# Kernel tuning notes

Measured on AMD Instinct MI355X. Metric: run time of the kernel, lower is better.

The kernel has to match this reference:

```python
import jax, jax.numpy as jnp
import numpy as np
import math

B, T, E = 16, 4096, 1024
WIN = 15
EPS = 1e-6
HALF = T // 2


def _make_linear(key, out_f, in_f):
    k1, k2 = jax.random.split(key)
    lim = 1.0 / math.sqrt(in_f)
    W = jax.random.uniform(k1, (out_f, in_f), minval=-lim, maxval=lim, dtype=jnp.float32)
    b = jax.random.uniform(k2, (out_f,), minval=-lim, maxval=lim, dtype=jnp.float32)
    return W, b


def setup_inputs() -> dict:
    key = jax.random.key(0)
    ks = jax.random.split(key, 5)
    x = jax.random.normal(ks[0], (B, T, E), dtype=jnp.float32)
    taper = jnp.linspace(1.0, 0.0, T, dtype=jnp.float32)
    cW1, cb1 = _make_linear(ks[1], HALF, T)
    cW2, cb2 = _make_linear(ks[2], HALF, HALF)
    pW1, pb1 = _make_linear(ks[3], HALF, T)
    pW2, pb2 = _make_linear(ks[4], HALF, HALF)
    return {"x": x, "taper": taper,
            "cW1": cW1, "cb1": cb1, "cW2": cW2, "cb2": cb2,
            "pW1": pW1, "pb1": pb1, "pW2": pW2, "pb2": pb2}


def _compressor(h, W1, b1, W2, b2):
    # Linear -> SiLU -> Linear -> Tanh  (torch Linear: y = h @ W^T + b)
    h = jax.nn.silu(h @ W1.T + b1)
    return jnp.tanh(h @ W2.T + b2)


def _tdiff_raw(c0):
    Bb, Tt = c0.shape
    xp = jnp.pad(c0, ((0, 0), (WIN, 0)))  # left pad with zeros
    num = jnp.zeros_like(c0)
    for d in range(1, WIN + 1):  # small fixed loop over window lags
        num = num + float(d) * jax.lax.dynamic_slice_in_dim(xp, WIN - d, Tt, axis=1)
    i = jnp.arange(Tt, dtype=jnp.float32)
    s = jnp.minimum(i, float(WIN))
    norm = s * (s + 1.0) * 0.5
    return jnp.where(norm > 0, num / jnp.maximum(norm, 1.0), 0.0)


def reference(x, taper, cW1, cb1, cW2, cb2, pW1, pb1, pW2, pb2):
    x_t = x * taper[None, :, None]          # (B,T,E) tapered in time
    c0 = x_t[..., 0]                         # (B,T)
    r = jnp.abs(c0) + EPS
    start = jnp.where(c0 >= 0, 0.0, jnp.float32(math.pi))
    v = jnp.clip(x_t[..., 1:] / r[..., None], -1.0 + EPS, 1.0 - EPS)
    phases = start + jnp.arcsin(v).sum(axis=-1)  # (B,T)
    tdiff = _compressor(_tdiff_raw(c0), pW1, pb1, pW2, pb2)   # (B,T/2)
    thash = _compressor(phases, cW1, cb1, cW2, cb2)           # (B,T/2)
    return jnp.stack([thash, tdiff], axis=-1)                 # (B,T/2,2)
```

## Files before the change

kernel.cpp:

```cpp
#include <hip/hip_runtime.h>
#include <math.h>

#define BB 16
#define TT 4096
#define EE 1024
#define HALF 2048
#define WIN 15
#define EPSF 1e-6f
#define PI_F   3.14159265358979323846f
#define PIO2_F 1.57079632679489662f

__device__ __forceinline__ float fast_asinf(float v) {
    float a  = fabsf(v);
    float z1 = a * a;
    float z2 = 0.5f * (1.0f - a);
    bool big = a > 0.5f;
    float z = big ? z2 : z1;
    float s = big ? sqrtf(z) : a;
    float p = fmaf(z, 4.2163199048e-2f, 2.4181311049e-2f);
    p = fmaf(z, p, 4.5470025998e-2f);
    p = fmaf(z, p, 7.4953002686e-2f);
    p = fmaf(z, p, 1.6666752422e-1f);
    float r = fmaf(s * z, p, s);
    float rb = fmaf(-2.0f, r, PIO2_F);
    r = big ? rb : r;
    return copysignf(r, v);
}

__global__ void phase_kernel(const float* __restrict__ x,
                             const float* __restrict__ taper,
                             float* __restrict__ phases_b,
                             float* __restrict__ c0_b) {
    const int wave = threadIdx.x >> 6;
    const int lane = threadIdx.x & 63;
    const int row  = blockIdx.x * 4 + wave;
    const int b = row >> 12;
    const int t = row & (TT - 1);
    const float tap = taper[t];
    const float* xr = x + (size_t)row * EE;

    const float c0 = xr[0] * tap;
    const float r = fabsf(c0) + EPSF;
    const float scale = tap / r;
    const float start = (c0 >= 0.0f) ? 0.0f : PI_F;
    const float LO = -1.0f + EPSF, HI = 1.0f - EPSF;

    const float4* xr4 = (const float4*)xr;
    float sum = 0.0f;
    #pragma unroll
    for (int j = 0; j < 4; ++j) {
        float4 v = xr4[j * 64 + lane];
        float a0 = fast_asinf(fminf(fmaxf(v.x * scale, LO), HI));
        if ((j | lane) == 0) a0 = 0.0f;
        sum += a0;
        sum += fast_asinf(fminf(fmaxf(v.y * scale, LO), HI));
        sum += fast_asinf(fminf(fmaxf(v.z * scale, LO), HI));
        sum += fast_asinf(fminf(fmaxf(v.w * scale, LO), HI));
    }
    #pragma unroll
    for (int off = 32; off > 0; off >>= 1)
        sum += __shfl_xor(sum, off, 64);

    if (lane == 0) {
        phases_b[b * TT + t] = start + sum;
        c0_b[b * TT + t]     = c0;
    }
}

__global__ void tdiff_kernel(const float* __restrict__ c0_b,
                             float* __restrict__ tdiff_b) {
    const int f = blockIdx.x * blockDim.x + threadIdx.x;
    if (f >= BB * TT) return;
    const int t = f & (TT - 1);
    float num = 0.0f;
    #pragma unroll
    for (int d = 1; d <= WIN; ++d) {
        if (d <= t) num += (float)d * c0_b[f - d];
    }
    const int s = (t < WIN) ? t : WIN;
    const float norm = 0.5f * (float)s * (float)(s + 1);
    tdiff_b[f] = (norm > 0.0f) ? (num / norm) : 0.0f;
}

__device__ __forceinline__ void gld_lds16(const float* g, float* l) {
    __builtin_amdgcn_global_load_lds(
        (const __attribute__((address_space(1))) unsigned int*)g,
        (__attribute__((address_space(3))) unsigned int*)l,
        16, 0, 0);
}

template <int K, int MODE>
__global__ void __launch_bounds__(256)
gemm_kernel(const float* __restrict__ A0, const float* __restrict__ W0,
            const float* __restrict__ bias0, float* __restrict__ out0,
            const float* __restrict__ A1, const float* __restrict__ W1,
            const float* __restrict__ bias1, float* __restrict__ out1) {
    constexpr int KT = 1024;
    constexpr int NT = K / KT;
    constexpr int LROW = KT + 4;
    __shared__ float als[16 * LROW];

    const int nb = HALF / 8;
    const int g = blockIdx.x / nb;
    const int obase = (blockIdx.x % nb) * 8;

    const float* A    = g ? A1 : A0;
    const float* W    = g ? W1 : W0;
    const float* bias = g ? bias1 : bias0;
    float* out        = g ? out1 : out0;

    const int wv   = threadIdx.x >> 6;
    const int lane = threadIdx.x & 63;
    const int col0 = obase + wv * 2;
    const int col1 = col0 + 1;
    const float* w0p = W + (size_t)col0 * K;
    const float* w1p = W + (size_t)col1 * K;

    float acc0[16], acc1[16];
    #pragma unroll
    for (int i = 0; i < 16; ++i) { acc0[i] = 0.0f; acc1[i] = 0.0f; }

    for (int t = 0; t < NT; ++t) {
        __syncthreads();
        #pragma unroll
        for (int i = 0; i < 4; ++i) {
            const int b = wv * 4 + i;
            const float* src = A + (size_t)b * K + t * KT + lane * 4;
            float* dst = &als[b * LROW];
            #pragma unroll
            for (int q = 0; q < 4; ++q)
                gld_lds16(src + q * 256, dst + q * 256);
        }
        __syncthreads();

        float4 w0[4], w1[4];
        #pragma unroll
        for (int s = 0; s < 4; ++s) {
            w0[s] = *(const float4*)(w0p + t * KT + s * 256 + lane * 4);
            w1[s] = *(const float4*)(w1p + t * KT + s * 256 + lane * 4);
        }

        #pragma unroll
        for (int s = 0; s < 4; ++s) {
            #pragma unroll
            for (int b = 0; b < 16; ++b) {
                const float4 a4 = *(const float4*)&als[b * LROW + s * 256 + lane * 4];
                acc0[b] += w0[s].x*a4.x + w0[s].y*a4.y + w0[s].z*a4.z + w0[s].w*a4.w;
                acc1[b] += w1[s].x*a4.x + w1[s].y*a4.y + w1[s].z*a4.z + w1[s].w*a4.w;
            }
        }
    }

    #pragma unroll
    for (int off = 32; off > 0; off >>= 1) {
        #pragma unroll
        for (int i = 0; i < 16; ++i) {
            acc0[i] += __shfl_xor(acc0[i], off, 64);
            acc1[i] += __shfl_xor(acc1[i], off, 64);
        }
    }

    const bool isw0 = (lane == 0), isw1 = (lane == 32);
    if (isw0 || isw1) {
        const int o = isw0 ? col0 : col1;
        const float bs = bias[o];
        #pragma unroll
        for (int i = 0; i < 16; ++i) {
            float s = (isw0 ? acc0[i] : acc1[i]) + bs;
            if (MODE == 0) {
                s = s / (1.0f + expf(-s));
                out[(size_t)i * HALF + o] = s;
            } else {
                s = tanhf(s);
                out[(size_t)i * (HALF * 2) + o * 2 + g] = s;
            }
        }
    }
}

extern "C" void kernel_launch(void* const* d_in, const int* in_sizes, int n_in,
                              void* d_out, int out_size, void* d_ws, size_t ws_size,
                              hipStream_t stream) {
    const float* x     = (const float*)d_in[0];
    const float* taper = (const float*)d_in[1];
    const float* cW1   = (const float*)d_in[2];
    const float* cb1   = (const float*)d_in[3];
    const float* cW2   = (const float*)d_in[4];
    const float* cb2   = (const float*)d_in[5];
    const float* pW1   = (const float*)d_in[6];
    const float* pb1   = (const float*)d_in[7];
    const float* pW2   = (const float*)d_in[8];
    const float* pb2   = (const float*)d_in[9];
    float* out = (float*)d_out;
    float* ws  = (float*)d_ws;

    float* phases_b = ws;
    float* c0_b     = ws + 65536;
    float* tdiff_b  = ws + 131072;
    float* H1_b     = ws + 196608;
    float* H2_b     = ws + 229376;

    phase_kernel<<<BB * TT / 4, 256, 0, stream>>>(x, taper, phases_b, c0_b);
    tdiff_kernel<<<BB * TT / 256, 256, 0, stream>>>(c0_b, tdiff_b);
    gemm_kernel<TT, 0><<<512, 256, 0, stream>>>(phases_b, cW1, cb1, H1_b,
                                                tdiff_b, pW1, pb1, H2_b);
    gemm_kernel<HALF, 1><<<512, 256, 0, stream>>>(H1_b, cW2, cb2, out,
                                                  H2_b, pW2, pb2, out);
}
```

Before: 108.5 us.

## Fuse tdiff and both GEMM stages into one cooperative kernel with grid sync

Replaces the three separate launches (tdiff, first-layer GEMM, second-layer GEMM) with one cooperative kernel of 512 blocks that runs the stages in sequence, separated by grid-wide barriers. The aim is to remove kernel launch gaps and the drain/ramp between dependent stages. If the cooperative launch fails, it falls back to the original separate launches. Grid syncs add their own barrier cost, and the fused kernel needs all 512 blocks resident at once, which constrains occupancy.

```diff
diff --git a/kernel.cpp b/kernel.cpp
--- a/kernel.cpp
+++ b/kernel.cpp
@@ -1,5 +1,8 @@
 #include <hip/hip_runtime.h>
+#include <hip/hip_cooperative_groups.h>
 #include <math.h>
+
+namespace cg = cooperative_groups;
 
 #define BB 16
 #define TT 4096
@@ -67,19 +70,20 @@
     }
 }
 
-__global__ void tdiff_kernel(const float* __restrict__ c0_b,
-                             float* __restrict__ tdiff_b) {
+__device__ __forceinline__ void stage_tdiff(const float* __restrict__ c0_b,
+                                            float* __restrict__ tdiff_b) {
     const int f = blockIdx.x * blockDim.x + threadIdx.x;
-    if (f >= BB * TT) return;
-    const int t = f & (TT - 1);
-    float num = 0.0f;
-    #pragma unroll
-    for (int d = 1; d <= WIN; ++d) {
-        if (d <= t) num += (float)d * c0_b[f - d];
-    }
-    const int s = (t < WIN) ? t : WIN;
-    const float norm = 0.5f * (float)s * (float)(s + 1);
-    tdiff_b[f] = (norm > 0.0f) ? (num / norm) : 0.0f;
+    if (f < BB * TT) {
+        const int t = f & (TT - 1);
+        float num = 0.0f;
+        #pragma unroll
+        for (int d = 1; d <= WIN; ++d) {
+            if (d <= t) num += (float)d * c0_b[f - d];
+        }
+        const int s = (t < WIN) ? t : WIN;
+        const float norm = 0.5f * (float)s * (float)(s + 1);
+        tdiff_b[f] = (norm > 0.0f) ? (num / norm) : 0.0f;
+    }
 }
 
 __device__ __forceinline__ void gld_lds16(const float* g, float* l) {
@@ -89,16 +93,20 @@
         16, 0, 0);
 }
 
+#define KT_G 1024
+#define LROW (KT_G + 4)
+
 template <int K, int MODE>
-__global__ void __launch_bounds__(256)
-gemm_kernel(const float* __restrict__ A0, const float* __restrict__ W0,
-            const float* __restrict__ bias0, float* __restrict__ out0,
-            const float* __restrict__ A1, const float* __restrict__ W1,
-            const float* __restrict__ bias1, float* __restrict__ out1) {
-    constexpr int KT = 1024;
-    constexpr int NT = K / KT;
-    constexpr int LROW = KT + 4;
-    __shared__ float als[16 * LROW];
+__device__ __forceinline__ void stage_gemm(const float* __restrict__ A0,
+                                           const float* __restrict__ W0,
+                                           const float* __restrict__ bias0,
+                                           float* out0,
+                                           const float* __restrict__ A1,
+                                           const float* __restrict__ W1,
+                                           const float* __restrict__ bias1,
+                                           float* out1,
+                                           float* als) {
+    constexpr int NT = K / KT_G;
 
     const int nb = HALF / 8;
     const int g = blockIdx.x / nb;
@@ -125,7 +133,7 @@
         #pragma unroll
         for (int i = 0; i < 4; ++i) {
             const int b = wv * 4 + i;
-            const float* src = A + (size_t)b * K + t * KT + lane * 4;
+            const float* src = A + (size_t)b * K + t * KT_G + lane * 4;
             float* dst = &als[b * LROW];
             #pragma unroll
             for (int q = 0; q < 4; ++q)
@@ -136,8 +144,8 @@
         float4 w0[4], w1[4];
         #pragma unroll
         for (int s = 0; s < 4; ++s) {
-            w0[s] = *(const float4*)(w0p + t * KT + s * 256 + lane * 4);
-            w1[s] = *(const float4*)(w1p + t * KT + s * 256 + lane * 4);
+            w0[s] = *(const float4*)(w0p + t * KT_G + s * 256 + lane * 4);
+            w1[s] = *(const float4*)(w1p + t * KT_G + s * 256 + lane * 4);
         }
 
         #pragma unroll
@@ -176,6 +184,33 @@
             }
         }
     }
+    __syncthreads();
+}
+
+__global__ void __launch_bounds__(256)
+mega_kernel(const float* phases_b, const float* c0_b, float* tdiff_b,
+            const float* cW1, const float* cb1, const float* cW2, const float* cb2,
+            const float* pW1, const float* pb1, const float* pW2, const float* pb2,
+            float* H1_b, float* H2_b, float* out) {
+    __shared__ float als[16 * LROW];
+    cg::grid_group grid = cg::this_grid();
+
+    stage_tdiff(c0_b, tdiff_b);
+    grid.sync();
+    stage_gemm<TT, 0>(phases_b, cW1, cb1, H1_b, tdiff_b, pW1, pb1, H2_b, als);
+    grid.sync();
+    stage_gemm<HALF, 1>(H1_b, cW2, cb2, out, H2_b, pW2, pb2, out, als);
+}
+
+__global__ void __launch_bounds__(256)
+k_tdiff(const float* c0_b, float* tdiff_b) { stage_tdiff(c0_b, tdiff_b); }
+
+template <int K, int MODE>
+__global__ void __launch_bounds__(256)
+k_gemm(const float* A0, const float* W0, const float* b0, float* o0,
+       const float* A1, const float* W1, const float* b1, float* o1) {
+    __shared__ float als[16 * LROW];
+    stage_gemm<K, MODE>(A0, W0, b0, o0, A1, W1, b1, o1, als);
 }
 
 extern "C" void kernel_launch(void* const* d_in, const int* in_sizes, int n_in,
@@ -201,9 +236,21 @@
     float* H2_b     = ws + 229376;
 
     phase_kernel<<<BB * TT / 4, 256, 0, stream>>>(x, taper, phases_b, c0_b);
-    tdiff_kernel<<<BB * TT / 256, 256, 0, stream>>>(c0_b, tdiff_b);
-    gemm_kernel<TT, 0><<<512, 256, 0, stream>>>(phases_b, cW1, cb1, H1_b,
-                                                tdiff_b, pW1, pb1, H2_b);
-    gemm_kernel<HALF, 1><<<512, 256, 0, stream>>>(H1_b, cW2, cb2, out,
-                                                  H2_b, pW2, pb2, out);
-}
+
+    void* args[] = {
+        (void*)&phases_b, (void*)&c0_b, (void*)&tdiff_b,
+        (void*)&cW1, (void*)&cb1, (void*)&cW2, (void*)&cb2,
+        (void*)&pW1, (void*)&pb1, (void*)&pW2, (void*)&pb2,
+        (void*)&H1_b, (void*)&H2_b, (void*)&out,
+    };
+    hipError_t e = hipLaunchCooperativeKernel((const void*)mega_kernel,
+                                              dim3(512), dim3(256), args, 0, stream);
+    if (e != hipSuccess) {
+        (void)hipGetLastError();
+        k_tdiff<<<256, 256, 0, stream>>>(c0_b, tdiff_b);
+        k_gemm<TT, 0><<<512, 256, 0, stream>>>(phases_b, cW1, cb1, H1_b,
+                                               tdiff_b, pW1, pb1, H2_b);
+        k_gemm<HALF, 1><<<512, 256, 0, stream>>>(H1_b, cW2, cb2, out,
+                                                 H2_b, pW2, pb2, out);
+    }
+}
```

New measurement: 210.1 us. +93.7%, slower.

## Fuse tdiff into phase kernel and double-buffer GEMM LDS staging

Applied to the files above, without the earlier changes.

Computes the triangular moving average inside the phase kernel by having lanes 1..15 load the lagged c0 values directly from x and reduce them with shuffles, removing the separate tdiff kernel and the c0 buffer. The first-layer GEMM now uses two LDS buffers with half-size K tiles, prefetching the next activation tile via global_load_lds while computing on the current one, synchronised with explicit vmcnt waits and barriers. This removes a launch and a serialized load/compute phase, at the cost of extra scattered loads per row and fragile manual waitcnt accounting.

```diff
diff --git a/kernel.cpp b/kernel.cpp
--- a/kernel.cpp
+++ b/kernel.cpp
@@ -27,10 +27,10 @@
     return copysignf(r, v);
 }
 
-__global__ void phase_kernel(const float* __restrict__ x,
-                             const float* __restrict__ taper,
-                             float* __restrict__ phases_b,
-                             float* __restrict__ c0_b) {
+__global__ void phase_tdiff_kernel(const float* __restrict__ x,
+                                   const float* __restrict__ taper,
+                                   float* __restrict__ phases_b,
+                                   float* __restrict__ tdiff_b) {
     const int wave = threadIdx.x >> 6;
     const int lane = threadIdx.x & 63;
     const int row  = blockIdx.x * 4 + wave;
@@ -38,6 +38,14 @@
     const int t = row & (TT - 1);
     const float tap = taper[t];
     const float* xr = x + (size_t)row * EE;
+
+    float xd = 0.0f, tapd = 0.0f;
+    const int td = t - lane;
+    const bool do_d = (lane >= 1) && (lane <= WIN) && (lane <= t);
+    if (do_d) {
+        xd   = x[((size_t)b * TT + td) * EE];
+        tapd = taper[td];
+    }
 
     const float c0 = xr[0] * tap;
     const float r = fabsf(c0) + EPSF;
@@ -61,25 +69,17 @@
     for (int off = 32; off > 0; off >>= 1)
         sum += __shfl_xor(sum, off, 64);
 
+    float contrib = do_d ? ((float)lane * xd * tapd) : 0.0f;
+    #pragma unroll
+    for (int off = 8; off > 0; off >>= 1)
+        contrib += __shfl_xor(contrib, off, 64);
+
     if (lane == 0) {
         phases_b[b * TT + t] = start + sum;
-        c0_b[b * TT + t]     = c0;
-    }
-}
-
-__global__ void tdiff_kernel(const float* __restrict__ c0_b,
-                             float* __restrict__ tdiff_b) {
-    const int f = blockIdx.x * blockDim.x + threadIdx.x;
-    if (f >= BB * TT) return;
-    const int t = f & (TT - 1);
-    float num = 0.0f;
-    #pragma unroll
-    for (int d = 1; d <= WIN; ++d) {
-        if (d <= t) num += (float)d * c0_b[f - d];
-    }
-    const int s = (t < WIN) ? t : WIN;
-    const float norm = 0.5f * (float)s * (float)(s + 1);
-    tdiff_b[f] = (norm > 0.0f) ? (num / norm) : 0.0f;
+        const int s = (t < WIN) ? t : WIN;
+        const float norm = 0.5f * (float)s * (float)(s + 1);
+        tdiff_b[b * TT + t] = (norm > 0.0f) ? (contrib / norm) : 0.0f;
+    }
 }
 
 __device__ __forceinline__ void gld_lds16(const float* g, float* l) {
@@ -95,10 +95,10 @@
             const float* __restrict__ bias0, float* __restrict__ out0,
             const float* __restrict__ A1, const float* __restrict__ W1,
             const float* __restrict__ bias1, float* __restrict__ out1) {
-    constexpr int KT = 1024;
+    constexpr int KT = 512;
     constexpr int NT = K / KT;
     constexpr int LROW = KT + 4;
-    __shared__ float als[16 * LROW];
+    __shared__ float als[2][16 * LROW];
 
     const int nb = HALF / 8;
     const int g = blockIdx.x / nb;
@@ -116,39 +116,53 @@
     const float* w0p = W + (size_t)col0 * K;
     const float* w1p = W + (size_t)col1 * K;
 
+    auto stage = [&](int t, int s) {
+        #pragma unroll
+        for (int i = 0; i < 4; ++i) {
+            const int br = wv * 4 + i;
+            const float* src = A + (size_t)br * K + t * KT + lane * 4;
+            float* dst = &als[s][br * LROW];
+            gld_lds16(src, dst);
+            gld_lds16(src + 256, dst + 256);
+        }
+    };
+
     float acc0[16], acc1[16];
     #pragma unroll
     for (int i = 0; i < 16; ++i) { acc0[i] = 0.0f; acc1[i] = 0.0f; }
 
+    stage(0, 0);
+
     for (int t = 0; t < NT; ++t) {
-        __syncthreads();
-        #pragma unroll
-        for (int i = 0; i < 4; ++i) {
-            const int b = wv * 4 + i;
-            const float* src = A + (size_t)b * K + t * KT + lane * 4;
-            float* dst = &als[b * LROW];
+        const int cur = t & 1;
+
+        float4 w0v[2], w1v[2];
+        #pragma unroll
+        for (int s2 = 0; s2 < 2; ++s2) {
+            w0v[s2] = *(const float4*)(w0p + t * KT + s2 * 256 + lane * 4);
+            w1v[s2] = *(const float4*)(w1p + t * KT + s2 * 256 + lane * 4);
+        }
+
+        if (t + 1 < NT) {
+            stage(t + 1, cur ^ 1);
+            asm volatile("s_waitcnt vmcnt(8)" ::: "memory");
+        } else {
+            asm volatile("s_waitcnt vmcnt(0)" ::: "memory");
+        }
+        __builtin_amdgcn_s_barrier();
+        __builtin_amdgcn_sched_barrier(0);
+
+        #pragma unroll
+        for (int s2 = 0; s2 < 2; ++s2) {
             #pragma unroll
-            for (int q = 0; q < 4; ++q)
-                gld_lds16(src + q * 256, dst + q * 256);
-        }
-        __syncthreads();
-
-        float4 w0[4], w1[4];
-        #pragma unroll
-        for (int s = 0; s < 4; ++s) {
-            w0[s] = *(const float4*)(w0p + t * KT + s * 256 + lane * 4);
-            w1[s] = *(const float4*)(w1p + t * KT + s * 256 + lane * 4);
-        }
-
-        #pragma unroll
-        for (int s = 0; s < 4; ++s) {
-            #pragma unroll
-            for (int b = 0; b < 16; ++b) {
-                const float4 a4 = *(const float4*)&als[b * LROW + s * 256 + lane * 4];
-                acc0[b] += w0[s].x*a4.x + w0[s].y*a4.y + w0[s].z*a4.z + w0[s].w*a4.w;
-                acc1[b] += w1[s].x*a4.x + w1[s].y*a4.y + w1[s].z*a4.z + w1[s].w*a4.w;
+            for (int br = 0; br < 16; ++br) {
+                const float4 a4 = *(const float4*)&als[cur][br * LROW + s2 * 256 + lane * 4];
+                acc0[br] += w0v[s2].x*a4.x + w0v[s2].y*a4.y + w0v[s2].z*a4.z + w0v[s2].w*a4.w;
+                acc1[br] += w1v[s2].x*a4.x + w1v[s2].y*a4.y + w1v[s2].z*a4.z + w1v[s2].w*a4.w;
             }
         }
+        __builtin_amdgcn_sched_barrier(0);
+        __builtin_amdgcn_s_barrier();
     }
 
     #pragma unroll
@@ -195,13 +209,11 @@
     float* ws  = (float*)d_ws;
 
     float* phases_b = ws;
-    float* c0_b     = ws + 65536;
-    float* tdiff_b  = ws + 131072;
-    float* H1_b     = ws + 196608;
-    float* H2_b     = ws + 229376;
-
-    phase_kernel<<<BB * TT / 4, 256, 0, stream>>>(x, taper, phases_b, c0_b);
-    tdiff_kernel<<<BB * TT / 256, 256, 0, stream>>>(c0_b, tdiff_b);
+    float* tdiff_b  = ws + 65536;
+    float* H1_b     = ws + 131072;
+    float* H2_b     = ws + 163840;
+
+    phase_tdiff_kernel<<<BB * TT / 4, 256, 0, stream>>>(x, taper, phases_b, tdiff_b);
     gemm_kernel<TT, 0><<<512, 256, 0, stream>>>(phases_b, cW1, cb1, H1_b,
                                                 tdiff_b, pW1, pb1, H2_b);
     gemm_kernel<HALF, 1><<<512, 256, 0, stream>>>(H1_b, cW2, cb2, out,
```

Measured after the change: 109.0 us. No clear change (+0.4%).
